# Optimization experiments

Measured on AMD Instinct MI355X. Metric: run time of the kernel, lower is better.

## Reference

```python
import jax, jax.numpy as jnp
import numpy as np

B, V, H, W = 2, 16, 512, 512
MAX_VARS, EMBED, P = 48, 1024, 8


def setup_inputs() -> dict:
    key = jax.random.key(0)
    k1, k2, k3, k4 = jax.random.split(key, 4)
    x = jax.random.normal(k1, (B, V, H, W), dtype=jnp.float32)
    vars_idx = jax.random.randint(k2, (V,), 0, MAX_VARS)
    # params scaled roughly like kaiming_uniform for fan_in = P*P
    bound = 1.0 / np.sqrt(P * P)
    proj_weights = jax.random.normal(k3, (MAX_VARS, EMBED, 1, P, P), dtype=jnp.float32) * bound
    proj_biases = jax.random.normal(k4, (MAX_VARS, EMBED), dtype=jnp.float32) * bound
    return {"x": x, "vars": vars_idx, "proj_weights": proj_weights, "proj_biases": proj_biases}


def reference(x, vars, proj_weights, proj_biases):
    # x: [B, V, H, W]; proj_weights: [max_vars, E, 1, p, p]; proj_biases: [max_vars, E]
    b, v, h_img, w_img = x.shape
    p = proj_weights.shape[-1]
    w_sel = proj_weights[vars][:, :, 0]          # [V, E, p, p]  (weight gather)
    b_sel = proj_biases[vars]                    # [V, E]
    hh, ww = h_img // p, w_img // p
    # non-overlapping patch extraction (stride == kernel) + per-variable matmul
    xp = x.reshape(b, v, hh, p, ww, p)           # [B, V, hh, p, ww, p]
    proj = jnp.einsum('bvhpwq,vepq->bvhwe', xp, w_sel)  # [B, V, hh, ww, E]
    # flatten=True: [B, V, L, E], L = hh*ww (matches reshape->flatten(3)->transpose(2,3))
    out = proj.reshape(b, v, hh * ww, -1) + b_sel[None, :, None, :]
    return out  # norm_layer=None -> Identity
```

## Files before the change

kernel.cpp:

```cpp
#include <hip/hip_runtime.h>

#define Bb 2
#define Vv 16
#define Hh 512
#define Ww 512
#define Kk 64
#define Ee 1024
#define Ll 4096

typedef __bf16 bf16x8 __attribute__((ext_vector_type(8)));
typedef float f32x4 __attribute__((ext_vector_type(4)));

static __device__ __forceinline__ bf16x8 cvt8(float4 a, float4 b) {
    bf16x8 r = { (__bf16)a.x, (__bf16)a.y, (__bf16)a.z, (__bf16)a.w,
                 (__bf16)b.x, (__bf16)b.y, (__bf16)b.z, (__bf16)b.w };
    return r;
}

__global__ __launch_bounds__(256) void patch_embed_kernel(
    const float* __restrict__ x, const int* __restrict__ vars,
    const float* __restrict__ pw, const float* __restrict__ pb,
    float* __restrict__ out)
{
    const int tid = threadIdx.x;
    const int mt  = blockIdx.x;
    const int bv  = blockIdx.y;
    const int v   = bv & (Vv - 1);
    const int var = vars[v];

    const int lane = tid & 63;
    const int wv   = tid >> 6;
    const int wE   = (wv >> 1) << 6;
    const int wL   = (wv & 1) << 6;
    const int ln   = lane & 15;
    const int quad = lane >> 4;

    bf16x8 xf[2][4];
    {
        const float* xb = x + ((size_t)bv * Hh + (size_t)mt * 16 + (wL >> 3) + quad) * Ww;
        #pragma unroll
        for (int kh = 0; kh < 2; kh++) {
            const float* xr = xb + (size_t)(kh * 4) * Ww;
            #pragma unroll
            for (int nj = 0; nj < 4; nj++) {
                const float4* p = (const float4*)(xr + (nj * 16 + ln) * 8);
                xf[kh][nj] = cvt8(p[0], p[1]);
            }
        }
    }

    const float* wb = pw + ((size_t)var * Ee + wE + ln) * Kk + quad * 8;
    const float* bb = pb + (size_t)var * Ee + wE + quad * 4;
    float* ob = out + (size_t)bv * Ll * Ee
                    + (size_t)(mt * 128 + wL + ln) * Ee + wE + quad * 4;

    float4 wraw[2][4][2];
    #pragma unroll
    for (int kh = 0; kh < 2; kh++)
        #pragma unroll
        for (int mi = 0; mi < 4; mi++) {
            const float4* p = (const float4*)(wb + (size_t)(mi * 16) * Kk + kh * 32);
            wraw[kh][mi][0] = p[0];
            wraw[kh][mi][1] = p[1];
        }

    #pragma unroll 1
    for (int nt = 0; nt < 8; nt++) {
        bf16x8 wf[2][4];
        #pragma unroll
        for (int kh = 0; kh < 2; kh++)
            #pragma unroll
            for (int mi = 0; mi < 4; mi++)
                wf[kh][mi] = cvt8(wraw[kh][mi][0], wraw[kh][mi][1]);

        f32x4 acc[4][4];
        #pragma unroll
        for (int mi = 0; mi < 4; mi++) {
            float4 t = *(const float4*)(bb + nt * 128 + mi * 16);
            f32x4 bias = { t.x, t.y, t.z, t.w };
            #pragma unroll
            for (int nj = 0; nj < 4; nj++) acc[mi][nj] = bias;
        }

        if (nt < 7) {
            #pragma unroll
            for (int kh = 0; kh < 2; kh++)
                #pragma unroll
                for (int mi = 0; mi < 4; mi++) {
                    const float4* p = (const float4*)(wb + (size_t)((nt + 1) * 128 + mi * 16) * Kk + kh * 32);
                    wraw[kh][mi][0] = p[0];
                    wraw[kh][mi][1] = p[1];
                }
        }

        #pragma unroll
        for (int kh = 0; kh < 2; kh++)
            #pragma unroll
            for (int mi = 0; mi < 4; mi++)
                #pragma unroll
                for (int nj = 0; nj < 4; nj++)
                    acc[mi][nj] = __builtin_amdgcn_mfma_f32_16x16x32_bf16(
                        wf[kh][mi], xf[kh][nj], acc[mi][nj], 0, 0, 0);

        #pragma unroll
        for (int nj = 0; nj < 4; nj++) {
            float* op = ob + (size_t)(nj * 16) * Ee + nt * 128;
            #pragma unroll
            for (int mi = 0; mi < 4; mi++)
                __builtin_nontemporal_store(acc[mi][nj], (f32x4*)(op + mi * 16));
        }
    }
}

extern "C" void kernel_launch(void* const* d_in, const int* in_sizes, int n_in,
                              void* d_out, int out_size, void* d_ws, size_t ws_size,
                              hipStream_t stream) {
    const float* x    = (const float*)d_in[0];
    const int*   vars = (const int*)d_in[1];
    const float* pw   = (const float*)d_in[2];
    const float* pb   = (const float*)d_in[3];
    float* out = (float*)d_out;
    dim3 grid(Ll / 128, Bb * Vv);
    dim3 block(256);
    hipLaunchKernelGGL(patch_embed_kernel, grid, block, 0, stream,
                       x, vars, pw, pb, out);
}
```

Before: 639.0 us.

## Move E-tile loop into grid dimension, one output tile per block

```diff
diff --git a/kernel.cpp b/kernel.cpp
--- a/kernel.cpp
+++ b/kernel.cpp
@@ -23,10 +23,10 @@
     float* __restrict__ out)
 {
     const int tid = threadIdx.x;
-    const int mt  = blockIdx.x;
-    const int bv  = blockIdx.y;
-    const int v   = bv & (Vv - 1);
-    const int var = vars[v];
+    const int nt  = blockIdx.x;
+    const int mt  = blockIdx.y;
+    const int bv  = blockIdx.z;
+    const int var = vars[bv & (Vv - 1)];
 
     const int lane = tid & 63;
     const int wv   = tid >> 6;
@@ -35,80 +35,59 @@
     const int ln   = lane & 15;
     const int quad = lane >> 4;
 
+    const float* xb = x + ((size_t)bv * Hh + (size_t)mt * 16 + (wL >> 3) + quad) * Ww;
     bf16x8 xf[2][4];
-    {
-        const float* xb = x + ((size_t)bv * Hh + (size_t)mt * 16 + (wL >> 3) + quad) * Ww;
+    #pragma unroll
+    for (int kh = 0; kh < 2; kh++) {
+        const float* xr = xb + (size_t)(kh * 4) * Ww;
         #pragma unroll
-        for (int kh = 0; kh < 2; kh++) {
-            const float* xr = xb + (size_t)(kh * 4) * Ww;
-            #pragma unroll
-            for (int nj = 0; nj < 4; nj++) {
-                const float4* p = (const float4*)(xr + (nj * 16 + ln) * 8);
-                xf[kh][nj] = cvt8(p[0], p[1]);
-            }
+        for (int nj = 0; nj < 4; nj++) {
+            const float4* p = (const float4*)(xr + (nj * 16 + ln) * 8);
+            float4 a = p[0], b = p[1];
+            xf[kh][nj] = cvt8(a, b);
         }
     }
 
-    const float* wb = pw + ((size_t)var * Ee + wE + ln) * Kk + quad * 8;
-    const float* bb = pb + (size_t)var * Ee + wE + quad * 4;
-    float* ob = out + (size_t)bv * Ll * Ee
-                    + (size_t)(mt * 128 + wL + ln) * Ee + wE + quad * 4;
+    const float* wb = pw + ((size_t)var * Ee + (size_t)nt * 128 + wE + ln) * Kk + quad * 8;
+    bf16x8 wf[2][4];
+    #pragma unroll
+    for (int kh = 0; kh < 2; kh++) {
+        #pragma unroll
+        for (int mi = 0; mi < 4; mi++) {
+            const float4* p = (const float4*)(wb + (size_t)(mi * 16) * Kk + kh * 32);
+            float4 a = p[0], b = p[1];
+            wf[kh][mi] = cvt8(a, b);
+        }
+    }
 
-    float4 wraw[2][4][2];
+    const float* bb = pb + (size_t)var * Ee + nt * 128 + wE + quad * 4;
+    f32x4 acc[4][4];
+    #pragma unroll
+    for (int mi = 0; mi < 4; mi++) {
+        float4 t = *(const float4*)(bb + mi * 16);
+        f32x4 bias = { t.x, t.y, t.z, t.w };
+        #pragma unroll
+        for (int nj = 0; nj < 4; nj++) acc[mi][nj] = bias;
+    }
+
     #pragma unroll
     for (int kh = 0; kh < 2; kh++)
         #pragma unroll
-        for (int mi = 0; mi < 4; mi++) {
-            const float4* p = (const float4*)(wb + (size_t)(mi * 16) * Kk + kh * 32);
-            wraw[kh][mi][0] = p[0];
-            wraw[kh][mi][1] = p[1];
-        }
+        for (int mi = 0; mi < 4; mi++)
+            #pragma unroll
+            for (int nj = 0; nj < 4; nj++)
+                acc[mi][nj] = __builtin_amdgcn_mfma_f32_16x16x32_bf16(
+                    wf[kh][mi], xf[kh][nj], acc[mi][nj], 0, 0, 0);
 
-    #pragma unroll 1
-    for (int nt = 0; nt < 8; nt++) {
-        bf16x8 wf[2][4];
+    float* ob = out + (size_t)bv * Ll * Ee
+                    + (size_t)(mt * 128 + wL + ln) * Ee
+                    + (size_t)nt * 128 + wE + quad * 4;
+    #pragma unroll
+    for (int nj = 0; nj < 4; nj++) {
+        float* op = ob + (size_t)(nj * 16) * Ee;
         #pragma unroll
-        for (int kh = 0; kh < 2; kh++)
-            #pragma unroll
-            for (int mi = 0; mi < 4; mi++)
-                wf[kh][mi] = cvt8(wraw[kh][mi][0], wraw[kh][mi][1]);
-
-        f32x4 acc[4][4];
-        #pragma unroll
-        for (int mi = 0; mi < 4; mi++) {
-            float4 t = *(const float4*)(bb + nt * 128 + mi * 16);
-            f32x4 bias = { t.x, t.y, t.z, t.w };
-            #pragma unroll
-            for (int nj = 0; nj < 4; nj++) acc[mi][nj] = bias;
-        }
-
-        if (nt < 7) {
-            #pragma unroll
-            for (int kh = 0; kh < 2; kh++)
-                #pragma unroll
-                for (int mi = 0; mi < 4; mi++) {
-                    const float4* p = (const float4*)(wb + (size_t)((nt + 1) * 128 + mi * 16) * Kk + kh * 32);
-                    wraw[kh][mi][0] = p[0];
-                    wraw[kh][mi][1] = p[1];
-                }
-        }
-
-        #pragma unroll
-        for (int kh = 0; kh < 2; kh++)
-            #pragma unroll
-            for (int mi = 0; mi < 4; mi++)
-                #pragma unroll
-                for (int nj = 0; nj < 4; nj++)
-                    acc[mi][nj] = __builtin_amdgcn_mfma_f32_16x16x32_bf16(
-                        wf[kh][mi], xf[kh][nj], acc[mi][nj], 0, 0, 0);
-
-        #pragma unroll
-        for (int nj = 0; nj < 4; nj++) {
-            float* op = ob + (size_t)(nj * 16) * Ee + nt * 128;
-            #pragma unroll
-            for (int mi = 0; mi < 4; mi++)
-                __builtin_nontemporal_store(acc[mi][nj], (f32x4*)(op + mi * 16));
-        }
+        for (int mi = 0; mi < 4; mi++)
+            __builtin_nontemporal_store(acc[mi][nj], (f32x4*)(op + mi * 16));
     }
 }
 
@@ -120,7 +99,7 @@
     const float* pw   = (const float*)d_in[2];
     const float* pb   = (const float*)d_in[3];
     float* out = (float*)d_out;
-    dim3 grid(Ll / 128, Bb * Vv);
+    dim3 grid(Ee / 128, Ll / 128, Bb * Vv);
     dim3 block(256);
     hipLaunchKernelGGL(patch_embed_kernel, grid, block, 0, stream,
                        x, vars, pw, pb, out);
```

Result: faster. 624.5 us (-2.3%).
